# Performance work log

Measured on AMD Instinct MI355X. Metric: run time of the kernel, lower is better.

Reference implementation:

```python
import jax, jax.numpy as jnp
import numpy as np

NUM_EMBEDDINGS = 8192
EMBEDDING_DIM = 512
COMMITMENT_COST = 0.25
N_INPUTS = 32768


def setup_inputs() -> dict:
    key = jax.random.key(0)
    k1, k2 = jax.random.split(key)
    inputs = jax.random.normal(k1, (N_INPUTS, EMBEDDING_DIM), dtype=jnp.float32)
    weight = jax.random.normal(k2, (NUM_EMBEDDINGS, EMBEDDING_DIM), dtype=jnp.float32)
    return {"inputs": inputs, "weight": weight}


def reference(inputs, weight):
    # distances[n, k] = ||x_n||^2 + ||w_k||^2 - 2 x_n . w_k   -> [N, K]
    distances = (
        jnp.sum(inputs ** 2, axis=1, keepdims=True)
        + jnp.sum(weight ** 2, axis=1)
        - 2.0 * (inputs @ weight.T)
    )
    probs = jax.nn.softmax(-distances, axis=-1)            # [N, K]
    idx = jnp.argmin(distances, axis=1)                    # [N]
    quantized = weight[idx]                                # gather == one-hot @ weight

    e_latent_loss = jnp.mean((jax.lax.stop_gradient(quantized) - inputs) ** 2)
    q_latent_loss = jnp.mean((quantized - jax.lax.stop_gradient(inputs)) ** 2)
    loss = q_latent_loss + COMMITMENT_COST * e_latent_loss

    # straight-through estimator
    quantized_st = inputs + jax.lax.stop_gradient(quantized - inputs)

    # avg over one-hot encodings == normalized code histogram
    counts = jnp.bincount(idx, length=NUM_EMBEDDINGS).astype(inputs.dtype)
    avg_probs = counts / inputs.shape[0]
    perplexity = jnp.exp(-jnp.sum(avg_probs * jnp.log(avg_probs + 1e-10)))

    return (quantized_st, probs, loss, perplexity)
```

## Files before the change

kernel.cpp:

```cpp
#include <hip/hip_runtime.h>
#include <hip/hip_fp16.h>
#include <math.h>

#define N_ROWS 32768
#define K_CODES 8192
#define DIM 512

#define OUT_Q 0
#define OUT_P ((size_t)N_ROWS * DIM)
#define OUT_LOSS (OUT_P + (size_t)N_ROWS * K_CODES)
#define OUT_PERP (OUT_LOSS + 1)

#define WS_WSQ 0
#define WS_CNT (K_CODES)
#define WS_ERR (2 * K_CODES)
#define WS_RED (2 * K_CODES + N_ROWS)
#define WS_F16 (WS_RED + 64)

#define XH_OFF ((size_t)0)
#define XL_OFF ((size_t)N_ROWS * DIM)
#define WH_OFF ((size_t)2 * N_ROWS * DIM)
#define WL_OFF ((size_t)2 * N_ROWS * DIM + (size_t)K_CODES * DIM)
#define F16_COUNT ((size_t)2 * (N_ROWS + K_CODES) * DIM)
#define WS_NEEDED ((size_t)WS_F16 * 4 + F16_COUNT * 2)

typedef _Float16 f16x8 __attribute__((ext_vector_type(8)));
typedef float f32x4 __attribute__((ext_vector_type(4)));
typedef float f32x2 __attribute__((ext_vector_type(2)));
typedef unsigned long long u64;

__device__ inline void load_lds16(const void* g, void* l) {
    __builtin_amdgcn_global_load_lds((const __attribute__((address_space(1))) void*)g,
                                     (__attribute__((address_space(3))) void*)l,
                                     16, 0, 0);
}

__device__ inline void ntstore4(float* p, f32x4 v) {
    __builtin_nontemporal_store(v, (f32x4*)p);
}

__device__ inline unsigned int fkey(float f) {
    unsigned int b = __float_as_uint(f);
    return b ^ ((unsigned int)((int)b >> 31) | 0x80000000u);
}
__device__ inline float fkey_inv(unsigned int k) {
    unsigned int b = (k & 0x80000000u) ? (k ^ 0x80000000u) : ~k;
    return __uint_as_float(b);
}

__global__ void wsq_kernel(const float* __restrict__ W, float* __restrict__ ws) {
    int row = blockIdx.x;
    int lane = threadIdx.x;
    const float* src = W + (size_t)row * DIM;
    float4 v0 = *(const float4*)(src + lane * 8);
    float4 v1 = *(const float4*)(src + lane * 8 + 4);
    float s = v0.x * v0.x + v0.y * v0.y + v0.z * v0.z + v0.w * v0.w
            + v1.x * v1.x + v1.y * v1.y + v1.z * v1.z + v1.w * v1.w;
#pragma unroll
    for (int off = 32; off > 0; off >>= 1) s += __shfl_down(s, off, 64);
    if (lane == 0) ws[WS_WSQ + row] = s;
}

__global__ void __launch_bounds__(256) convert_split_kernel(
    const float* __restrict__ X, const float* __restrict__ W,
    _Float16* __restrict__ f16base, float* __restrict__ ws) {
    const size_t NX8 = (size_t)N_ROWS * DIM / 8;
    size_t t = (size_t)blockIdx.x * 256 + threadIdx.x;
    const float* src;
    _Float16 *hd, *ld;
    bool isW = (t >= NX8);
    if (!isW) {
        src = X + t * 8;
        hd = f16base + XH_OFF + t * 8;
        ld = f16base + XL_OFF + t * 8;
    } else {
        size_t u = t - NX8;
        src = W + u * 8;
        hd = f16base + WH_OFF + u * 8;
        ld = f16base + WL_OFF + u * 8;
    }
    float4 v0 = *(const float4*)src;
    float4 v1 = *(const float4*)(src + 4);
    float v[8] = {v0.x, v0.y, v0.z, v0.w, v1.x, v1.y, v1.z, v1.w};
    f16x8 h, l;
    float s = 0.f;
#pragma unroll
    for (int i = 0; i < 8; ++i) {
        _Float16 hv = (_Float16)v[i];
        h[i] = hv;
        l[i] = (_Float16)(v[i] - (float)hv);
        s += v[i] * v[i];
    }
    *(f16x8*)hd = h;
    *(f16x8*)ld = l;
    if (isW) {
#pragma unroll
        for (int off = 32; off > 0; off >>= 1) s += __shfl_down(s, off, 64);
        if ((threadIdx.x & 63) == 0) ws[WS_WSQ + ((t - NX8) >> 6)] = s;
    }
}

#define LDSB 24576
#define AH_O 0
#define AL_O 8192
#define BH_O 16384
#define BL_O 20480

__global__ void __launch_bounds__(512, 2) gemm_dist_mfma_kernel(
    const _Float16* __restrict__ f16base, const float* __restrict__ ws,
    float* __restrict__ out) {
    __shared__ __align__(16) _Float16 lds[3 * LDSB];

    const int tid = threadIdx.x;
    const int w = tid >> 6;
    const int lane = tid & 63;

    int lin = blockIdx.y * 64 + blockIdx.x;
    int swz = (lin & 7) * 1024 + (lin >> 3);
    const int bn = (swz & 63) * 128;
    const int bm = (swz >> 6) * 256;

    const int wr = w >> 1;
    const int wc = w & 1;
    const int q = lane >> 4;
    const int fm = lane & 15;
    const int l4 = lane >> 2;
    const int p = lane & 3;

    f32x4 acc[4][4];
#pragma unroll
    for (int i = 0; i < 4; ++i)
#pragma unroll
        for (int j = 0; j < 4; ++j) acc[i][j] = (f32x4){0.f, 0.f, 0.f, 0.f};

    auto stage = [&](int ks, _Float16* buf, int part) {
        const int kk = ks * 32;
        int g = w * 2 + part;
        int arow = g * 16 + l4;
        int ca = p ^ ((arow >> 1) & 3);
        size_t aoff = (size_t)(bm + arow) * DIM + kk + ca * 8;
        load_lds16(f16base + XH_OFF + aoff, buf + AH_O + g * 512);
        load_lds16(f16base + XL_OFF + aoff, buf + AL_O + g * 512);
        int brow = w * 16 + l4;
        int cb = p ^ ((brow >> 1) & 3);
        size_t boff = (size_t)(bn + brow) * DIM + kk + cb * 8;
        if (part == 0)
            load_lds16(f16base + WH_OFF + boff, buf + BH_O + w * 512);
        else
            load_lds16(f16base + WL_OFF + boff, buf + BL_O + w * 512);
    };

    _Float16* c0 = lds;
    _Float16* c1 = lds + LDSB;
    _Float16* c2 = lds + 2 * LDSB;

    stage(0, c0, 0); stage(0, c0, 1);
    stage(1, c1, 0); stage(1, c1, 1);
    asm volatile("s_waitcnt vmcnt(6)" ::: "memory");
    __builtin_amdgcn_s_barrier();
    __builtin_amdgcn_sched_barrier(0);

#pragma unroll 1
    for (int ks = 0; ks < 16; ++ks) {
        f16x8 bhv[4], blv[4];
#pragma unroll
        for (int j = 0; j < 4; ++j) {
            int bb = wc * 64 + j * 16 + fm;
            int off = bb * 32 + ((q ^ ((bb >> 1) & 3)) * 8);
            bhv[j] = *(const f16x8*)&c0[BH_O + off];
            blv[j] = *(const f16x8*)&c0[BL_O + off];
        }
        f16x8 ah[2], al[2];
#pragma unroll
        for (int i = 0; i < 2; ++i) {
            int am = wr * 64 + i * 16 + fm;
            int off = am * 32 + ((q ^ ((am >> 1) & 3)) * 8);
            ah[i] = *(const f16x8*)&c0[AH_O + off];
            al[i] = *(const f16x8*)&c0[AL_O + off];
        }
        if (ks < 14) stage(ks + 2, c2, 0);
        __builtin_amdgcn_s_setprio(1);
#pragma unroll
        for (int i = 0; i < 2; ++i)
#pragma unroll
            for (int j = 0; j < 4; ++j) {
                acc[i][j] = __builtin_amdgcn_mfma_f32_16x16x32_f16(
                    ah[i], bhv[j], acc[i][j], 0, 0, 0);
                acc[i][j] = __builtin_amdgcn_mfma_f32_16x16x32_f16(
                    ah[i], blv[j], acc[i][j], 0, 0, 0);
                acc[i][j] = __builtin_amdgcn_mfma_f32_16x16x32_f16(
                    al[i], bhv[j], acc[i][j], 0, 0, 0);
            }
        __builtin_amdgcn_s_setprio(0);
        __builtin_amdgcn_s_barrier();

#pragma unroll
        for (int i = 0; i < 2; ++i) {
            int am = wr * 64 + (i + 2) * 16 + fm;
            int off = am * 32 + ((q ^ ((am >> 1) & 3)) * 8);
            ah[i] = *(const f16x8*)&c0[AH_O + off];
            al[i] = *(const f16x8*)&c0[AL_O + off];
        }
        if (ks < 14) stage(ks + 2, c2, 1);
        __builtin_amdgcn_s_setprio(1);
#pragma unroll
        for (int i = 0; i < 2; ++i)
#pragma unroll
            for (int j = 0; j < 4; ++j) {
                acc[i + 2][j] = __builtin_amdgcn_mfma_f32_16x16x32_f16(
                    ah[i], bhv[j], acc[i + 2][j], 0, 0, 0);
                acc[i + 2][j] = __builtin_amdgcn_mfma_f32_16x16x32_f16(
                    ah[i], blv[j], acc[i + 2][j], 0, 0, 0);
                acc[i + 2][j] = __builtin_amdgcn_mfma_f32_16x16x32_f16(
                    al[i], bhv[j], acc[i + 2][j], 0, 0, 0);
            }
        __builtin_amdgcn_s_setprio(0);
        if (ks < 14) {
            asm volatile("s_waitcnt vmcnt(6)" ::: "memory");
        } else if (ks == 14) {
            asm volatile("s_waitcnt vmcnt(0)" ::: "memory");
        }
        __builtin_amdgcn_s_barrier();
        __builtin_amdgcn_sched_barrier(0);

        _Float16* t0 = c0; c0 = c1; c1 = c2; c2 = t0;
    }

    const float* wsq = ws + WS_WSQ;
    float* Dout = out + OUT_P;
    const int q4 = q * 4;
#pragma unroll
    for (int i = 0; i < 4; ++i) {
#pragma unroll
        for (int j = 0; j < 4; ++j) {
            int n = bn + wc * 64 + j * 16 + fm;
            float wn = wsq[n];
#pragma unroll
            for (int r = 0; r < 4; ++r) {
                int m = bm + wr * 64 + i * 16 + q4 + r;
                Dout[(size_t)m * K_CODES + n] = wn - 2.f * acc[i][j][r];
            }
        }
    }
}

#define BM 128
#define BN 128
#define BK 16

__global__ void __launch_bounds__(256) gemm_dist_fp32_kernel(
    const float* __restrict__ X, const float* __restrict__ W,
    const float* __restrict__ ws, float* __restrict__ out) {
    __shared__ float As[BK][BM];
    __shared__ float Bs[BK][BN];

    const int bn = blockIdx.x * BN;
    const int bm = blockIdx.y * BM;
    const int tid = threadIdx.x;
    const int tx = tid & 15;
    const int ty = tid >> 4;
    const int lr = tid >> 1;
    const int lc = (tid & 1) * 8;

    float acc[8][8];
#pragma unroll
    for (int i = 0; i < 8; ++i)
#pragma unroll
        for (int j = 0; j < 8; ++j) acc[i][j] = 0.f;

    const float* aptr = X + (size_t)(bm + lr) * DIM + lc;
    const float* bptr = W + (size_t)(bn + lr) * DIM + lc;

    for (int k0 = 0; k0 < DIM; k0 += BK) {
        float4 a0 = *(const float4*)(aptr + k0);
        float4 a1 = *(const float4*)(aptr + k0 + 4);
        float4 b0 = *(const float4*)(bptr + k0);
        float4 b1 = *(const float4*)(bptr + k0 + 4);
        __syncthreads();
        As[lc + 0][lr] = a0.x; As[lc + 1][lr] = a0.y;
        As[lc + 2][lr] = a0.z; As[lc + 3][lr] = a0.w;
        As[lc + 4][lr] = a1.x; As[lc + 5][lr] = a1.y;
        As[lc + 6][lr] = a1.z; As[lc + 7][lr] = a1.w;
        Bs[lc + 0][lr] = b0.x; Bs[lc + 1][lr] = b0.y;
        Bs[lc + 2][lr] = b0.z; Bs[lc + 3][lr] = b0.w;
        Bs[lc + 4][lr] = b1.x; Bs[lc + 5][lr] = b1.y;
        Bs[lc + 6][lr] = b1.z; Bs[lc + 7][lr] = b1.w;
        __syncthreads();
#pragma unroll
        for (int kk = 0; kk < BK; ++kk) {
            float a[8], b[8];
            *(float4*)&a[0] = *(const float4*)&As[kk][ty * 8];
            *(float4*)&a[4] = *(const float4*)&As[kk][ty * 8 + 4];
            *(float4*)&b[0] = *(const float4*)&Bs[kk][tx * 8];
            *(float4*)&b[4] = *(const float4*)&Bs[kk][tx * 8 + 4];
#pragma unroll
            for (int i = 0; i < 8; ++i)
#pragma unroll
                for (int j = 0; j < 8; ++j)
                    acc[i][j] = fmaf(a[i], b[j], acc[i][j]);
        }
    }

    const float* wsq = ws + WS_WSQ;
    const int m0 = bm + ty * 8;
    const int n0 = bn + tx * 8;
    float wn[8];
    *(float4*)&wn[0] = *(const float4*)(wsq + n0);
    *(float4*)&wn[4] = *(const float4*)(wsq + n0 + 4);
    float* Dout = out + OUT_P;
#pragma unroll
    for (int i = 0; i < 8; ++i) {
        float4 o0, o1;
        o0.x = wn[0] - 2.f * acc[i][0];
        o0.y = wn[1] - 2.f * acc[i][1];
        o0.z = wn[2] - 2.f * acc[i][2];
        o0.w = wn[3] - 2.f * acc[i][3];
        o1.x = wn[4] - 2.f * acc[i][4];
        o1.y = wn[5] - 2.f * acc[i][5];
        o1.z = wn[6] - 2.f * acc[i][6];
        o1.w = wn[7] - 2.f * acc[i][7];
        float* drow = Dout + (size_t)(m0 + i) * K_CODES + n0;
        *(float4*)(drow) = o0;
        *(float4*)(drow + 4) = o1;
    }
}

__global__ void __launch_bounds__(256) probs_quant_kernel(
    const float* __restrict__ X, const float* __restrict__ W,
    float* __restrict__ out, float* __restrict__ ws) {
    const int tid = threadIdx.x;
    const int wv = tid >> 6;
    const int rA = blockIdx.x;
    const int rB = blockIdx.x + N_ROWS / 2;
    __shared__ u64 mred[4];
    __shared__ float sred[4];
    __shared__ float ered[4];

    const float* DA = out + OUT_P + (size_t)rA * K_CODES;
    const float* DB = out + OUT_P + (size_t)rB * K_CODES;

    f32x2 xA = ((const f32x2*)(X + (size_t)rA * DIM))[tid];
    f32x2 xB = ((const f32x2*)(X + (size_t)rB * DIM))[tid];

    f32x4 eA[8];
#pragma unroll
    for (int t = 0; t < 8; ++t)
        eA[t] = *(const f32x4*)(DA + (tid + t * 256) * 4);

    u64 bestA = ~0ull;
#pragma unroll
    for (int t = 0; t < 8; ++t) {
        unsigned int c0 = (unsigned int)((tid + t * 256) * 4);
#pragma unroll
        for (int c = 0; c < 4; ++c) {
            u64 k = ((u64)fkey(eA[t][c]) << 32) | (c0 + c);
            bestA = k < bestA ? k : bestA;
        }
    }
#pragma unroll
    for (int d = 1; d < 64; d <<= 1) {
        u64 o = __shfl_xor(bestA, d, 64);
        bestA = o < bestA ? o : bestA;
    }
    if ((tid & 63) == 0) mred[wv] = bestA;
    __syncthreads();
    u64 bmA = mred[0];
#pragma unroll
    for (int i = 1; i < 4; ++i) bmA = mred[i] < bmA ? mred[i] : bmA;
    const float sminA = fkey_inv((unsigned int)(bmA >> 32));
    const int aminA = (int)(bmA & 0xFFFFFFFFu);

    f32x4 eB[8];
#pragma unroll
    for (int t = 0; t < 8; ++t)
        eB[t] = *(const f32x4*)(DB + (tid + t * 256) * 4);

    float sumA = 0.f;
#pragma unroll
    for (int t = 0; t < 8; ++t) {
#pragma unroll
        for (int c = 0; c < 4; ++c) {
            float v = __expf(sminA - eA[t][c]);
            eA[t][c] = v;
            sumA += v;
        }
    }
#pragma unroll
    for (int off = 32; off > 0; off >>= 1) sumA += __shfl_down(sumA, off, 64);
    if ((tid & 63) == 0) sred[wv] = sumA;
    __syncthreads();
    const float invA = 1.0f / (sred[0] + sred[1] + sred[2] + sred[3]);

    float* DAw = out + OUT_P + (size_t)rA * K_CODES;
#pragma unroll
    for (int t = 0; t < 8; ++t) {
        f32x4 v = eA[t];
        v *= invA;
        ntstore4(DAw + (tid + t * 256) * 4, v);
    }

    {
        f32x2 wq = ((const f32x2*)(W + (size_t)aminA * DIM))[tid];
        f32x2 d = wq - xA;
        f32x2 o = xA + d;
        __builtin_nontemporal_store(
            o, (f32x2*)(out + OUT_Q + (size_t)rA * DIM) + tid);
        float err = d.x * d.x + d.y * d.y;
#pragma unroll
        for (int off = 32; off > 0; off >>= 1) err += __shfl_down(err, off, 64);
        if ((tid & 63) == 0) ered[wv] = err;
        __syncthreads();
        if (tid == 0) {
            ws[WS_ERR + rA] = ered[0] + ered[1] + ered[2] + ered[3];
            atomicAdd(ws + WS_CNT + aminA, 1.0f);
        }
    }

    u64 bestB = ~0ull;
#pragma unroll
    for (int t = 0; t < 8; ++t) {
        unsigned int c0 = (unsigned int)((tid + t * 256) * 4);
#pragma unroll
        for (int c = 0; c < 4; ++c) {
            u64 k = ((u64)fkey(eB[t][c]) << 32) | (c0 + c);
            bestB = k < bestB ? k : bestB;
        }
    }
#pragma unroll
    for (int d = 1; d < 64; d <<= 1) {
        u64 o = __shfl_xor(bestB, d, 64);
        bestB = o < bestB ? o : bestB;
    }
    if ((tid & 63) == 0) mred[wv] = bestB;
    __syncthreads();
    u64 bmB = mred[0];
#pragma unroll
    for (int i = 1; i < 4; ++i) bmB = mred[i] < bmB ? mred[i] : bmB;
    const float sminB = fkey_inv((unsigned int)(bmB >> 32));
    const int aminB = (int)(bmB & 0xFFFFFFFFu);

    float sumB = 0.f;
#pragma unroll
    for (int t = 0; t < 8; ++t) {
#pragma unroll
        for (int c = 0; c < 4; ++c) {
            float v = __expf(sminB - eB[t][c]);
            eB[t][c] = v;
            sumB += v;
        }
    }
#pragma unroll
    for (int off = 32; off > 0; off >>= 1) sumB += __shfl_down(sumB, off, 64);
    if ((tid & 63) == 0) sred[wv] = sumB;
    __syncthreads();
    const float invB = 1.0f / (sred[0] + sred[1] + sred[2] + sred[3]);

    float* DBw = out + OUT_P + (size_t)rB * K_CODES;
#pragma unroll
    for (int t = 0; t < 8; ++t) {
        f32x4 v = eB[t];
        v *= invB;
        ntstore4(DBw + (tid + t * 256) * 4, v);
    }

    {
        f32x2 wq = ((const f32x2*)(W + (size_t)aminB * DIM))[tid];
        f32x2 d = wq - xB;
        f32x2 o = xB + d;
        __builtin_nontemporal_store(
            o, (f32x2*)(out + OUT_Q + (size_t)rB * DIM) + tid);
        float err = d.x * d.x + d.y * d.y;
#pragma unroll
        for (int off = 32; off > 0; off >>= 1) err += __shfl_down(err, off, 64);
        if ((tid & 63) == 0) ered[wv] = err;
        __syncthreads();
        if (tid == 0) {
            ws[WS_ERR + rB] = ered[0] + ered[1] + ered[2] + ered[3];
            atomicAdd(ws + WS_CNT + aminB, 1.0f);
        }
    }
}

__global__ void __launch_bounds__(256) finalize_part_kernel(
    float* __restrict__ ws) {
    __shared__ float red[256];
    const int b = blockIdx.x;
    const int tid = threadIdx.x;

    float errsum = 0.f;
    const int ebase = b * 1024;
#pragma unroll
    for (int j = tid; j < 1024; j += 256) errsum += ws[WS_ERR + ebase + j];

    float p = ws[WS_CNT + b * 256 + tid] * (1.0f / (float)N_ROWS);
    float ent = -p * logf(p + 1e-10f);

    red[tid] = errsum;
    __syncthreads();
    for (int st = 128; st > 0; st >>= 1) {
        if (tid < st) red[tid] += red[tid + st];
        __syncthreads();
    }
    if (tid == 0) ws[WS_RED + b] = red[0];
    __syncthreads();
    red[tid] = ent;
    __syncthreads();
    for (int st = 128; st > 0; st >>= 1) {
        if (tid < st) red[tid] += red[tid + st];
        __syncthreads();
    }
    if (tid == 0) ws[WS_RED + 32 + b] = red[0];
}

__global__ void __launch_bounds__(64) finalize_fin_kernel(
    float* __restrict__ out, const float* __restrict__ ws) {
    const int tid = threadIdx.x;
    float ev = tid < 32 ? ws[WS_RED + tid] : 0.f;
    float nv = tid < 32 ? ws[WS_RED + 32 + tid] : 0.f;
#pragma unroll
    for (int off = 32; off > 0; off >>= 1) {
        ev += __shfl_down(ev, off, 64);
        nv += __shfl_down(nv, off, 64);
    }
    if (tid == 0) {
        float mse = ev * (1.0f / ((float)N_ROWS * (float)DIM));
        out[OUT_LOSS] = mse + 0.25f * mse;
        out[OUT_PERP] = expf(nv);
    }
}

extern "C" void kernel_launch(void* const* d_in, const int* in_sizes, int n_in,
                              void* d_out, int out_size, void* d_ws, size_t ws_size,
                              hipStream_t stream) {
    const float* X = (const float*)d_in[0];
    const float* W = (const float*)d_in[1];
    float* out = (float*)d_out;
    float* ws = (float*)d_ws;

    hipMemsetAsync(ws + WS_CNT, 0, K_CODES * sizeof(float), stream);

    if (ws_size >= WS_NEEDED) {
        _Float16* f16base = (_Float16*)(ws + WS_F16);
        const int conv_blocks =
            (int)(((size_t)(N_ROWS + K_CODES) * DIM / 8 + 255) / 256);
        convert_split_kernel<<<conv_blocks, 256, 0, stream>>>(X, W, f16base, ws);

        dim3 ggrid(64, 128);
        gemm_dist_mfma_kernel<<<ggrid, 512, 0, stream>>>(f16base, ws, out);
    } else {
        wsq_kernel<<<K_CODES, 64, 0, stream>>>(W, ws);
        dim3 ggrid(K_CODES / BN, N_ROWS / BM);
        gemm_dist_fp32_kernel<<<ggrid, 256, 0, stream>>>(X, W, ws, out);
    }

    probs_quant_kernel<<<N_ROWS / 2, 256, 0, stream>>>(X, W, out, ws);
    finalize_part_kernel<<<32, 256, 0, stream>>>(ws);
    finalize_fin_kernel<<<1, 64, 0, stream>>>(out, ws);
}
```

Baseline: 2.277 ms.

## Fuse softmax/argmin/quantize epilogue into GEMM via last-block-per-panel atomic counter

After each GEMM tile writes its distance values, the block increments a per-row-panel atomic counter. The last of the 64 blocks covering a 256-row panel then runs the softmax, argmin, quantize and error reduction for those rows. Rows are processed with double-buffered loads, and the separate probs_quant kernel launch is removed on the MFMA path. The goal is to overlap the epilogue with other blocks' GEMM work and read the distance rows while they may still be in cache. The cost is that a single 512-thread block serially handles 256 rows of 8192 values, which can leave a long tail at the end of the kernel.

```diff
diff --git a/kernel.cpp b/kernel.cpp
--- a/kernel.cpp
+++ b/kernel.cpp
@@ -15,7 +15,8 @@
 #define WS_CNT (K_CODES)
 #define WS_ERR (2 * K_CODES)
 #define WS_RED (2 * K_CODES + N_ROWS)
-#define WS_F16 (WS_RED + 64)
+#define WS_PANEL (WS_RED + 64)
+#define WS_F16 (WS_PANEL + 128)
 
 #define XH_OFF ((size_t)0)
 #define XL_OFF ((size_t)N_ROWS * DIM)
@@ -107,7 +108,8 @@
 #define BL_O 20480
 
 __global__ void __launch_bounds__(512, 2) gemm_dist_mfma_kernel(
-    const _Float16* __restrict__ f16base, const float* __restrict__ ws,
+    const _Float16* __restrict__ f16base, const float* __restrict__ X,
+    const float* __restrict__ W, float* __restrict__ ws,
     float* __restrict__ out) {
     __shared__ __align__(16) _Float16 lds[3 * LDSB];
 
@@ -242,6 +244,105 @@
             }
         }
     }
+
+    __threadfence();
+    __syncthreads();
+    unsigned* panel = (unsigned*)(ws + WS_PANEL);
+    unsigned* ovp = (unsigned*)lds + 32;
+    if (tid == 0) ovp[0] = atomicAdd(panel + (bm >> 8), 1u);
+    __syncthreads();
+    if (ovp[0] != 63u) return;
+
+    {
+        u64* mredv = (u64*)lds;
+        float* sredv = (float*)lds + 16;
+        float* eredv = (float*)lds + 24;
+        float* Dbase = out + OUT_P;
+
+        f32x4 eC[4], eN[4];
+        auto LOADROW = [&](f32x4* e, int row) {
+            const float* Dr = Dbase + (size_t)row * K_CODES;
+#pragma unroll
+            for (int t = 0; t < 4; ++t)
+                e[t] = *(const f32x4*)(Dr + (tid + t * 512) * 4);
+        };
+        auto PROC = [&](f32x4* e, int row) {
+            u64 best = ~0ull;
+#pragma unroll
+            for (int t = 0; t < 4; ++t) {
+                unsigned c0i = (unsigned)((tid + t * 512) * 4);
+#pragma unroll
+                for (int c = 0; c < 4; ++c) {
+                    u64 k = ((u64)fkey(e[t][c]) << 32) | (c0i + c);
+                    best = k < best ? k : best;
+                }
+            }
+#pragma unroll
+            for (int d = 1; d < 64; d <<= 1) {
+                u64 o = __shfl_xor(best, d, 64);
+                best = o < best ? o : best;
+            }
+            if (lane == 0) mredv[w] = best;
+            __syncthreads();
+            u64 bmk = mredv[0];
+#pragma unroll
+            for (int i2 = 1; i2 < 8; ++i2) bmk = mredv[i2] < bmk ? mredv[i2] : bmk;
+            const float smin = fkey_inv((unsigned)(bmk >> 32));
+            const int amin = (int)(bmk & 0xFFFFFFFFu);
+            float xv = X[(size_t)row * DIM + tid];
+            float wqv = W[(size_t)amin * DIM + tid];
+            float sum = 0.f;
+#pragma unroll
+            for (int t = 0; t < 4; ++t) {
+#pragma unroll
+                for (int c = 0; c < 4; ++c) {
+                    float v = __expf(smin - e[t][c]);
+                    e[t][c] = v;
+                    sum += v;
+                }
+            }
+#pragma unroll
+            for (int off = 32; off > 0; off >>= 1)
+                sum += __shfl_down(sum, off, 64);
+            if (lane == 0) sredv[w] = sum;
+            __syncthreads();
+            float tot = sredv[0];
+#pragma unroll
+            for (int i2 = 1; i2 < 8; ++i2) tot += sredv[i2];
+            const float inv = 1.0f / tot;
+            float* Dw = Dbase + (size_t)row * K_CODES;
+#pragma unroll
+            for (int t = 0; t < 4; ++t) {
+                f32x4 v = e[t];
+                v *= inv;
+                ntstore4(Dw + (tid + t * 512) * 4, v);
+            }
+            float dq = wqv - xv;
+            out[OUT_Q + (size_t)row * DIM + tid] = xv + dq;
+            float err = dq * dq;
+#pragma unroll
+            for (int off = 32; off > 0; off >>= 1)
+                err += __shfl_down(err, off, 64);
+            if (lane == 0) eredv[w] = err;
+            __syncthreads();
+            if (tid == 0) {
+                float e8 = eredv[0];
+#pragma unroll
+                for (int i2 = 1; i2 < 8; ++i2) e8 += eredv[i2];
+                ws[WS_ERR + row] = e8;
+                atomicAdd(ws + WS_CNT + amin, 1.0f);
+            }
+        };
+
+        LOADROW(eC, bm);
+#pragma unroll 1
+        for (int r = 0; r < 256; r += 2) {
+            LOADROW(eN, bm + r + 1);
+            PROC(eC, bm + r);
+            if (r + 2 < 256) LOADROW(eC, bm + r + 2);
+            PROC(eN, bm + r + 1);
+        }
+    }
 }
 
 #define BM 128
@@ -538,6 +639,7 @@
     float* ws = (float*)d_ws;
 
     hipMemsetAsync(ws + WS_CNT, 0, K_CODES * sizeof(float), stream);
+    hipMemsetAsync(ws + WS_PANEL, 0, 128 * sizeof(float), stream);
 
     if (ws_size >= WS_NEEDED) {
         _Float16* f16base = (_Float16*)(ws + WS_F16);
@@ -546,14 +648,14 @@
         convert_split_kernel<<<conv_blocks, 256, 0, stream>>>(X, W, f16base, ws);
 
         dim3 ggrid(64, 128);
-        gemm_dist_mfma_kernel<<<ggrid, 512, 0, stream>>>(f16base, ws, out);
+        gemm_dist_mfma_kernel<<<ggrid, 512, 0, stream>>>(f16base, X, W, ws, out);
     } else {
         wsq_kernel<<<K_CODES, 64, 0, stream>>>(W, ws);
         dim3 ggrid(K_CODES / BN, N_ROWS / BM);
         gemm_dist_fp32_kernel<<<ggrid, 256, 0, stream>>>(X, W, ws, out);
-    }
-
-    probs_quant_kernel<<<N_ROWS / 2, 256, 0, stream>>>(X, W, out, ws);
+        probs_quant_kernel<<<N_ROWS / 2, 256, 0, stream>>>(X, W, out, ws);
+    }
+
     finalize_part_kernel<<<32, 256, 0, stream>>>(ws);
     finalize_fin_kernel<<<1, 64, 0, stream>>>(out, ws);
 }
```

New measurement: 5.504 ms. 2.42x slower.
